# Performance work log

Hardware: AMD Instinct MI355X
Metric: run time of the kernel (lower is better)

The kernel has to match this reference:

```python
import jax, jax.numpy as jnp
import numpy as np

N_NODES = 100000
N_EDGES = 3200000
IN_F, HID, OUT_F = 256, 128, 8


def gcn_conv(x, src, dst, W, b, n_nodes):
    # PyG GCNConv: linear transform, add self-loops, symmetric normalization, scatter-add, bias
    x = x @ W  # [N, F_out]
    loop = jnp.arange(n_nodes, dtype=src.dtype)
    src_f = jnp.concatenate([src, loop])
    dst_f = jnp.concatenate([dst, loop])
    ones = jnp.ones(src_f.shape[0], dtype=x.dtype)
    deg = jax.ops.segment_sum(ones, dst_f, num_segments=n_nodes)  # in-degree incl self-loop
    dinv = jax.lax.rsqrt(jnp.maximum(deg, 1e-12))
    norm = dinv[src_f] * dinv[dst_f]  # [E+N]
    msgs = x[src_f] * norm[:, None]
    out = jax.ops.segment_sum(msgs, dst_f, num_segments=n_nodes)
    return out + b


def setup_inputs() -> dict:
    key = jax.random.key(0)
    k1, k2, k3, k4 = jax.random.split(key, 4)
    x = jax.random.normal(k1, (N_NODES, IN_F), dtype=jnp.float32)
    edge_index = jax.random.randint(k2, (2, N_EDGES), 0, N_NODES, dtype=jnp.int64)
    W1 = jax.random.normal(k3, (IN_F, HID), dtype=jnp.float32) * (1.0 / np.sqrt(IN_F))
    b1 = jnp.zeros((HID,), dtype=jnp.float32)
    W2 = jax.random.normal(k4, (HID, OUT_F), dtype=jnp.float32) * (1.0 / np.sqrt(HID))
    b2 = jnp.zeros((OUT_F,), dtype=jnp.float32)
    return {"x": x, "edge_index": edge_index, "W1": W1, "b1": b1, "W2": W2, "b2": b2}


def reference(x, edge_index, W1, b1, W2, b2):
    n_nodes = x.shape[0]
    src, dst = edge_index[0], edge_index[1]
    h = gcn_conv(x, src, dst, W1, b1, n_nodes)
    h = jax.nn.relu(h)
    h = gcn_conv(h, src, dst, W2, b2, n_nodes)
    return jax.nn.log_softmax(h, axis=1)
```

## Files before the change

### kernel.cpp

```cpp
#include <hip/hip_runtime.h>
#include <hip/hip_bf16.h>
#include <stdint.h>

#define N_NODES 100000
#define N_EDGES 3200000
#define IN_F 256
#define HID 128
#define OUT_F 8

#define NB   391
#define PASS 6144
#define CAP  10240
#define BCAP 9216

typedef short short8 __attribute__((ext_vector_type(8)));
typedef float f32x4 __attribute__((ext_vector_type(4)));
typedef float f32x2 __attribute__((ext_vector_type(2)));


__device__ __forceinline__ uint32_t pk_bf16(float a, float b) {
    uint32_t ua = __float_as_uint(a);
    uint32_t ub = __float_as_uint(b);
    ua = (ua + 0x7fff + ((ua >> 16) & 1)) >> 16;
    ub = (ub + 0x7fff + ((ub >> 16) & 1)) & 0xffff0000u;
    return ua | ub;
}

__global__ __launch_bounds__(512) void k_part(const int* __restrict__ src,
                                              const int* __restrict__ dst,
                                              int* __restrict__ gcur,
                                              uint32_t* __restrict__ epk, int E) {
    __shared__ int lcntA[NB], lcntB[NB], lcnt[NB], loff[NB], ladj[NB], lcur[NB];
    __shared__ int sc[512];
    __shared__ uint32_t stage[PASS];
    int tid = threadIdx.x;
    int e0 = blockIdx.x * PASS;
    int nE = E - e0; if (nE > PASS) nE = PASS;
    int n4 = nE >> 2;

    for (int i = tid; i < NB; i += 512) { lcntA[i] = 0; lcntB[i] = 0; lcur[i] = 0; }
    __syncthreads();
    const int4* d4 = (const int4*)(dst + e0);
    const int4* s4 = (const int4*)(src + e0);
    {
        int* lc = ((tid >> 6) & 1) ? lcntB : lcntA;
        for (int i = tid; i < n4; i += 512) {
            int4 d = d4[i];
            atomicAdd(&lc[d.x >> 8], 1);
            atomicAdd(&lc[d.y >> 8], 1);
            atomicAdd(&lc[d.z >> 8], 1);
            atomicAdd(&lc[d.w >> 8], 1);
        }
    }
    __syncthreads();
    int v = 0;
    if (tid < NB) { v = lcntA[tid] + lcntB[tid]; lcnt[tid] = v; }
    sc[tid] = v;
    __syncthreads();
    for (int d = 1; d < 512; d <<= 1) {
        int t = (tid >= d) ? sc[tid - d] : 0;
        __syncthreads();
        sc[tid] += t;
        __syncthreads();
    }
    if (tid < NB) loff[tid] = sc[tid] - v;
    __syncthreads();
    if (tid < NB) {
        int len = lcnt[tid];
        if (len > 0) ladj[tid] = atomicAdd(&gcur[tid * 64], len);
    }
    __syncthreads();
    for (int i = tid; i < n4; i += 512) {
        int4 s = s4[i];
        int4 d = d4[i];
        int b0 = d.x >> 8, b1 = d.y >> 8, b2 = d.z >> 8, b3 = d.w >> 8;
        int r0 = atomicAdd(&lcur[b0], 1);
        int r1 = atomicAdd(&lcur[b1], 1);
        int r2 = atomicAdd(&lcur[b2], 1);
        int r3 = atomicAdd(&lcur[b3], 1);
        stage[loff[b0] + r0] = (uint32_t)s.x | ((uint32_t)(d.x & 255) << 17);
        stage[loff[b1] + r1] = (uint32_t)s.y | ((uint32_t)(d.y & 255) << 17);
        stage[loff[b2] + r2] = (uint32_t)s.z | ((uint32_t)(d.z & 255) << 17);
        stage[loff[b3] + r3] = (uint32_t)s.w | ((uint32_t)(d.w & 255) << 17);
    }
    __syncthreads();
    int wv = tid >> 6, ln = tid & 63;
    int sub = ln >> 4, l16 = ln & 15;
    for (int b = wv * 4 + sub; b < NB; b += 32) {
        int len = lcnt[b];
        if (len) {
            int lo = loff[b];
            uint32_t* dstp = epk + (size_t)b * BCAP + ladj[b];
            for (int j = l16; j < len; j += 16) dstp[j] = stage[lo + j];
        }
    }
}

__global__ __launch_bounds__(1024) void k_csr(const uint32_t* __restrict__ epk,
                                              const int* __restrict__ gcur,
                                              int* __restrict__ offs,
                                              int* __restrict__ cnt,
                                              float* __restrict__ dinv,
                                              int* __restrict__ ssrc, int N) {
    __shared__ int lcntP[4][256], lcur[256], loff[256];
    __shared__ uint32_t stage[CAP];
    int tid = threadIdx.x, b = blockIdx.x;
    size_t base = (size_t)b * BCAP;
    int m = gcur[b * 64];
    const uint32_t* ep = epk + base;

    if (tid < 256) { lcntP[0][tid] = 0; lcntP[1][tid] = 0; lcntP[2][tid] = 0; lcntP[3][tid] = 0; }
    __syncthreads();
    {
        int* lc = lcntP[(tid >> 6) & 3];
        for (int i = tid; i < m; i += 1024)
            atomicAdd(&lc[(ep[i] >> 17) & 255], 1);
    }
    __syncthreads();
    int v = 0;
    if (tid < 256) {
        v = lcntP[0][tid] + lcntP[1][tid] + lcntP[2][tid] + lcntP[3][tid];
        loff[tid] = v;
    }
    __syncthreads();
    for (int d = 1; d < 256; d <<= 1) {
        int t = (tid >= d && tid < 256) ? loff[tid - d] : 0;
        __syncthreads();
        if (tid < 256) loff[tid] += t;
        __syncthreads();
    }
    int excl = (tid < 256) ? (loff[tid] - v) : 0;
    __syncthreads();
    if (tid < 256) {
        loff[tid] = excl;
        lcur[tid] = 0;
        int node = b * 256 + tid;
        if (node < N) {
            offs[node] = (int)base + excl;
            cnt[node] = v;
            dinv[node] = rsqrtf((float)(v + 1));
        }
    }
    __syncthreads();
    if (m <= CAP) {
        for (int i = tid; i < m; i += 1024) {
            uint32_t u = ep[i];
            int ld = (u >> 17) & 255;
            int r = atomicAdd(&lcur[ld], 1);
            stage[loff[ld] + r] = u & 0x1FFFF;
        }
        __syncthreads();
        for (int i = tid; i < m; i += 1024) ssrc[base + i] = (int)stage[i];
    } else {
        for (int i = tid; i < m; i += 1024) {
            uint32_t u = ep[i];
            int ld = (u >> 17) & 255;
            int r = atomicAdd(&lcur[ld], 1);
            ssrc[base + loff[ld] + r] = (int)(u & 0x1FFFF);
        }
    }
}

__global__ __launch_bounds__(256) void k_wcast(const float* __restrict__ W1,
                                               ushort* __restrict__ Wbf) {
    __shared__ ushort T[128][33];
    int t = threadIdx.x;
    int k0 = blockIdx.x * 32;
    for (int idx = t; idx < 32 * 128; idx += 256) {
        int k = idx >> 7, n = idx & 127;
        uint32_t uv = __float_as_uint(W1[(size_t)(k0 + k) * HID + n]);
        uv = (uv + 0x7fff + ((uv >> 16) & 1)) >> 16;
        T[n][k] = (ushort)uv;
    }
    __syncthreads();
    for (int idx = t; idx < 32 * 128; idx += 256) {
        int n = idx >> 5, k = idx & 31;
        Wbf[(size_t)n * IN_F + k0 + k] = T[n][k];
    }
}

__global__ __launch_bounds__(256) void k_gemm1(const float* __restrict__ X,
                                               const ushort* __restrict__ Wbf,
                                               const float* __restrict__ dinv,
                                               uint32_t* __restrict__ Hs8, int M) {
    __shared__ uint32_t As[64 * 20];
    __shared__ uint32_t Bs[128 * 20];
    int t = threadIdx.x;
    int lane = t & 63, w = t >> 6;
    int q = lane >> 4, c16 = lane & 15;
    int row0 = blockIdx.x * 64;

    int ar = t >> 2, a4 = (t & 3);
    int grow = row0 + ar; if (grow >= M) grow = M - 1;
    const float* xrow = X + (size_t)grow * IN_F;
    int bn = t >> 1, b1h = (t & 1);
    const ushort* wrow = Wbf + (size_t)bn * IN_F;

    f32x4 acc[8];
    #pragma unroll
    for (int j = 0; j < 8; j++) acc[j] = (f32x4){0.f, 0.f, 0.f, 0.f};

    for (int kc = 0; kc < IN_F; kc += 32) {
        float4 x0 = *(const float4*)(xrow + kc + a4 * 8);
        float4 x1 = *(const float4*)(xrow + kc + a4 * 8 + 4);
        uint4 wv0 = *(const uint4*)(wrow + kc + b1h * 16);
        uint4 wv1 = *(const uint4*)(wrow + kc + b1h * 16 + 8);
        __syncthreads();
        *(uint2*)&As[ar * 20 + a4 * 4]     = make_uint2(pk_bf16(x0.x, x0.y), pk_bf16(x0.z, x0.w));
        *(uint2*)&As[ar * 20 + a4 * 4 + 2] = make_uint2(pk_bf16(x1.x, x1.y), pk_bf16(x1.z, x1.w));
        *(uint4*)&Bs[bn * 20 + b1h * 8]     = wv0;
        *(uint4*)&Bs[bn * 20 + b1h * 8 + 4] = wv1;
        __syncthreads();
        short8 af = *(const short8*)&As[(w * 16 + c16) * 20 + q * 4];
        #pragma unroll
        for (int j = 0; j < 8; j++) {
            short8 bf = *(const short8*)&Bs[(j * 16 + c16) * 20 + q * 4];
            acc[j] = __builtin_amdgcn_mfma_f32_16x16x32_bf16(af, bf, acc[j], 0, 0, 0);
        }
    }
    float dv[4];
    #pragma unroll
    for (int r = 0; r < 4; r++) {
        int gr = row0 + w * 16 + q * 4 + r;
        dv[r] = (gr < M) ? dinv[gr] : 0.f;
    }
    #pragma unroll
    for (int r = 0; r < 4; r++) {
        int gr = row0 + w * 16 + q * 4 + r;
        uint32_t lo = 0, hi = 0;
        lo = __builtin_amdgcn_cvt_pk_fp8_f32(acc[0][r] * dv[r], acc[1][r] * dv[r], lo, false);
        lo = __builtin_amdgcn_cvt_pk_fp8_f32(acc[2][r] * dv[r], acc[3][r] * dv[r], lo, true);
        hi = __builtin_amdgcn_cvt_pk_fp8_f32(acc[4][r] * dv[r], acc[5][r] * dv[r], hi, false);
        hi = __builtin_amdgcn_cvt_pk_fp8_f32(acc[6][r] * dv[r], acc[7][r] * dv[r], hi, true);
        if (gr < M) *(uint2*)&Hs8[(size_t)gr * 32 + c16 * 2] = make_uint2(lo, hi);
    }
}

__global__ __launch_bounds__(256) void k_agg1(const uint32_t* __restrict__ hs,
                                              const int* __restrict__ offs,
                                              const int* __restrict__ cnt,
                                              const float* __restrict__ dinv,
                                              const int* __restrict__ ssrc,
                                              const float* __restrict__ b1,
                                              const float* __restrict__ W2,
                                              uint32_t* __restrict__ h2bf, int N) {
    __shared__ float w2t[OUT_F * HID];
    __shared__ float b1p[HID];
    int t = threadIdx.x;
    for (int i = t; i < OUT_F * HID; i += 256) {
        int f = i >> 7, rem = i & 127;
        int cc = rem >> 2, bb = rem & 3;
        int feat = ((cc & 1) * 4 + bb) * 16 + (cc >> 1);
        w2t[i] = W2[feat * OUT_F + f];
    }
    if (t < HID) {
        int cc = t >> 2, bb = t & 3;
        b1p[t] = b1[((cc & 1) * 4 + bb) * 16 + (cc >> 1)];
    }
    __syncthreads();
    int wid = (blockIdx.x * 256 + t) >> 6;
    int lane = t & 63;
    if (wid >= N) return;
    int h = lane >> 5, c = lane & 31;
    float dv = dinv[wid];
    f32x2 s01 = {0.f, 0.f}, s23 = {0.f, 0.f};
    if (h == 0) {
        uint32_t u = hs[(size_t)wid * 32 + c];
        s01 = __builtin_amdgcn_cvt_pk_f32_fp8(u, false);
        s23 = __builtin_amdgcn_cvt_pk_f32_fp8(u, true);
    }
    int beg = offs[wid], n = cnt[wid];
    const int* sp = ssrc + beg;
    int j = h;
    for (; j + 14 < n; j += 16) {
        int e0 = sp[j],      e1 = sp[j + 2],  e2 = sp[j + 4],  e3 = sp[j + 6];
        int e4 = sp[j + 8],  e5 = sp[j + 10], e6 = sp[j + 12], e7 = sp[j + 14];
        uint32_t u0 = hs[(size_t)e0 * 32 + c];
        uint32_t u1 = hs[(size_t)e1 * 32 + c];
        uint32_t u2 = hs[(size_t)e2 * 32 + c];
        uint32_t u3 = hs[(size_t)e3 * 32 + c];
        uint32_t u4 = hs[(size_t)e4 * 32 + c];
        uint32_t u5 = hs[(size_t)e5 * 32 + c];
        uint32_t u6 = hs[(size_t)e6 * 32 + c];
        uint32_t u7 = hs[(size_t)e7 * 32 + c];
        s01 += __builtin_amdgcn_cvt_pk_f32_fp8(u0, false); s23 += __builtin_amdgcn_cvt_pk_f32_fp8(u0, true);
        s01 += __builtin_amdgcn_cvt_pk_f32_fp8(u1, false); s23 += __builtin_amdgcn_cvt_pk_f32_fp8(u1, true);
        s01 += __builtin_amdgcn_cvt_pk_f32_fp8(u2, false); s23 += __builtin_amdgcn_cvt_pk_f32_fp8(u2, true);
        s01 += __builtin_amdgcn_cvt_pk_f32_fp8(u3, false); s23 += __builtin_amdgcn_cvt_pk_f32_fp8(u3, true);
        s01 += __builtin_amdgcn_cvt_pk_f32_fp8(u4, false); s23 += __builtin_amdgcn_cvt_pk_f32_fp8(u4, true);
        s01 += __builtin_amdgcn_cvt_pk_f32_fp8(u5, false); s23 += __builtin_amdgcn_cvt_pk_f32_fp8(u5, true);
        s01 += __builtin_amdgcn_cvt_pk_f32_fp8(u6, false); s23 += __builtin_amdgcn_cvt_pk_f32_fp8(u6, true);
        s01 += __builtin_amdgcn_cvt_pk_f32_fp8(u7, false); s23 += __builtin_amdgcn_cvt_pk_f32_fp8(u7, true);
    }
    for (; j + 6 < n; j += 8) {
        int e0 = sp[j], e1 = sp[j + 2], e2 = sp[j + 4], e3 = sp[j + 6];
        uint32_t u0 = hs[(size_t)e0 * 32 + c];
        uint32_t u1 = hs[(size_t)e1 * 32 + c];
        uint32_t u2 = hs[(size_t)e2 * 32 + c];
        uint32_t u3 = hs[(size_t)e3 * 32 + c];
        s01 += __builtin_amdgcn_cvt_pk_f32_fp8(u0, false); s23 += __builtin_amdgcn_cvt_pk_f32_fp8(u0, true);
        s01 += __builtin_amdgcn_cvt_pk_f32_fp8(u1, false); s23 += __builtin_amdgcn_cvt_pk_f32_fp8(u1, true);
        s01 += __builtin_amdgcn_cvt_pk_f32_fp8(u2, false); s23 += __builtin_amdgcn_cvt_pk_f32_fp8(u2, true);
        s01 += __builtin_amdgcn_cvt_pk_f32_fp8(u3, false); s23 += __builtin_amdgcn_cvt_pk_f32_fp8(u3, true);
    }
    for (; j < n; j += 2) {
        uint32_t u = hs[(size_t)sp[j] * 32 + c];
        s01 += __builtin_amdgcn_cvt_pk_f32_fp8(u, false);
        s23 += __builtin_amdgcn_cvt_pk_f32_fp8(u, true);
    }
    s01[0] += __shfl_xor(s01[0], 32);
    s01[1] += __shfl_xor(s01[1], 32);
    s23[0] += __shfl_xor(s23[0], 32);
    s23[1] += __shfl_xor(s23[1], 32);
    float4 bb = *(const float4*)(b1p + c * 4);
    float o0 = fmaxf(fmaf(s01[0], dv, bb.x), 0.f);
    float o1 = fmaxf(fmaf(s01[1], dv, bb.y), 0.f);
    float o2 = fmaxf(fmaf(s23[0], dv, bb.z), 0.f);
    float o3 = fmaxf(fmaf(s23[1], dv, bb.w), 0.f);
    int f0 = h * 4;
    float p[4];
    #pragma unroll
    for (int f = 0; f < 4; f++) {
        float4 wv = *(const float4*)&w2t[(f0 + f) * HID + c * 4];
        p[f] = o0 * wv.x + o1 * wv.y + o2 * wv.z + o3 * wv.w;
    }
    #pragma unroll
    for (int d = 1; d < 32; d <<= 1) {
        #pragma unroll
        for (int f = 0; f < 4; f++) p[f] += __shfl_xor(p[f], d);
    }
    if (c == 0) {
        uint32_t w0 = pk_bf16(p[0] * dv, p[1] * dv);
        uint32_t w1 = pk_bf16(p[2] * dv, p[3] * dv);
        *(uint2*)&h2bf[(size_t)wid * 4 + h * 2] = make_uint2(w0, w1);
    }
}

__global__ __launch_bounds__(256) void k_agg2(const uint32_t* __restrict__ h2bf,
                                              const int* __restrict__ offs,
                                              const int* __restrict__ cnt,
                                              const float* __restrict__ dinv,
                                              const int* __restrict__ ssrc,
                                              const float* __restrict__ b2,
                                              float* __restrict__ out, int N) {
    int wid = (blockIdx.x * 256 + threadIdx.x) >> 6;
    int lane = threadIdx.x & 63;
    if (wid >= N) return;
    int f2 = lane & 3, g = lane >> 2;
    float dv = dinv[wid];
    int beg = offs[wid], n = cnt[wid];
    const int* sp = ssrc + beg;
    float a0 = 0.f, a1 = 0.f;
    int j = g;
    for (; j + 48 < n; j += 64) {
        int s0 = sp[j], s1 = sp[j + 16], s2 = sp[j + 32], s3 = sp[j + 48];
        uint32_t v0 = h2bf[(size_t)s0 * 4 + f2];
        uint32_t v1 = h2bf[(size_t)s1 * 4 + f2];
        uint32_t v2 = h2bf[(size_t)s2 * 4 + f2];
        uint32_t v3 = h2bf[(size_t)s3 * 4 + f2];
        a0 += __uint_as_float(v0 << 16) + __uint_as_float(v1 << 16)
            + __uint_as_float(v2 << 16) + __uint_as_float(v3 << 16);
        a1 += __uint_as_float(v0 & 0xffff0000u) + __uint_as_float(v1 & 0xffff0000u)
            + __uint_as_float(v2 & 0xffff0000u) + __uint_as_float(v3 & 0xffff0000u);
    }
    for (; j < n; j += 16) {
        uint32_t v = h2bf[(size_t)sp[j] * 4 + f2];
        a0 += __uint_as_float(v << 16);
        a1 += __uint_as_float(v & 0xffff0000u);
    }
    a0 += __shfl_xor(a0, 4);  a1 += __shfl_xor(a1, 4);
    a0 += __shfl_xor(a0, 8);  a1 += __shfl_xor(a1, 8);
    a0 += __shfl_xor(a0, 16); a1 += __shfl_xor(a1, 16);
    a0 += __shfl_xor(a0, 32); a1 += __shfl_xor(a1, 32);
    uint32_t vs = h2bf[(size_t)wid * 4 + f2];
    a0 += __uint_as_float(vs << 16);
    a1 += __uint_as_float(vs & 0xffff0000u);
    float acc0 = fmaf(a0, dv, b2[f2 * 2]);
    float acc1 = fmaf(a1, dv, b2[f2 * 2 + 1]);
    float m = fmaxf(acc0, acc1);
    m = fmaxf(m, __shfl_xor(m, 1));
    m = fmaxf(m, __shfl_xor(m, 2));
    float e = expf(acc0 - m) + expf(acc1 - m);
    e += __shfl_xor(e, 1);
    e += __shfl_xor(e, 2);
    float ls = logf(e);
    if (g == 0) {
        float2 r = make_float2(acc0 - m - ls, acc1 - m - ls);
        *(float2*)&out[(size_t)wid * OUT_F + f2 * 2] = r;
    }
}

extern "C" void kernel_launch(void* const* d_in, const int* in_sizes, int n_in,
                              void* d_out, int out_size, void* d_ws, size_t ws_size,
                              hipStream_t stream) {
    const float* x   = (const float*)d_in[0];
    const int*   ei  = (const int*)d_in[1];
    const float* W1  = (const float*)d_in[2];
    const float* b1  = (const float*)d_in[3];
    const float* W2  = (const float*)d_in[4];
    const float* b2  = (const float*)d_in[5];
    float* out = (float*)d_out;

    const int N = N_NODES, E = N_EDGES;
    const int* src = ei;
    const int* dst = ei + E;

    char* p = (char*)d_ws;
    auto carve = [&](size_t bytes) -> void* {
        void* r = (void*)p;
        p += (bytes + 511) & ~(size_t)511;
        return r;
    };
    int*      gcur  = (int*)carve((size_t)NB * 64 * 4);
    uint32_t* epk   = (uint32_t*)carve((size_t)NB * BCAP * 4);
    int*      offs  = (int*)carve((size_t)N * 4);
    int*      cnt   = (int*)carve((size_t)N * 4);
    float*    dinv  = (float*)carve((size_t)N * 4);
    int*      ssrc  = (int*)carve((size_t)NB * BCAP * 4);
    ushort*   wbf   = (ushort*)carve((size_t)HID * IN_F * 2);
    uint32_t* hs8   = (uint32_t*)carve((size_t)N * 32 * 4);
    uint32_t* h2bf  = (uint32_t*)carve((size_t)N * 4 * 4);

    hipMemsetAsync(gcur, 0, (size_t)NB * 64 * 4, stream);

    k_wcast<<<8, 256, 0, stream>>>(W1, wbf);
    k_part<<<(E + PASS - 1) / PASS, 512, 0, stream>>>(src, dst, gcur, epk, E);
    k_csr<<<NB, 1024, 0, stream>>>(epk, gcur, offs, cnt, dinv, ssrc, N);

    k_gemm1<<<(N + 63) / 64, 256, 0, stream>>>(x, wbf, dinv, hs8, N);
    k_agg1<<<(N * 64 + 255) / 256, 256, 0, stream>>>(hs8, offs, cnt, dinv, ssrc, b1, W2, h2bf, N);
    k_agg2<<<(N * 64 + 255) / 256, 256, 0, stream>>>(h2bf, offs, cnt, dinv, ssrc, b2, out, N);
}
```

Measured before the change: 345.3 us.

## Split layer-1 aggregation into four feature-slice passes with atomic partial projection

Layer-1 aggregation now runs as four sequential block passes, each gathering only a 32-byte slice of every neighbor's 128-byte fp8 row, with 8 edges in flight per wave instead of 2. The aim is to shrink the gathered working set per pass so it fits in cache better. Each pass atomically adds its partial W2 projection into a float buffer, and a new finalize kernel scales and packs that buffer to bf16. The cost is reading the index lists four times, plus an extra memset, atomics and one more kernel launch.

```diff
diff --git a/kernel.cpp b/kernel.cpp
--- a/kernel.cpp
+++ b/kernel.cpp
@@ -12,6 +12,7 @@
 #define PASS 6144
 #define CAP  10240
 #define BCAP 9216
+#define NPP  25000
 
 typedef short short8 __attribute__((ext_vector_type(8)));
 typedef float f32x4 __attribute__((ext_vector_type(4)));
@@ -236,104 +237,103 @@
     }
 }
 
-__global__ __launch_bounds__(256) void k_agg1(const uint32_t* __restrict__ hs,
-                                              const int* __restrict__ offs,
-                                              const int* __restrict__ cnt,
-                                              const float* __restrict__ dinv,
-                                              const int* __restrict__ ssrc,
-                                              const float* __restrict__ b1,
-                                              const float* __restrict__ W2,
-                                              uint32_t* __restrict__ h2bf, int N) {
-    __shared__ float w2t[OUT_F * HID];
+__global__ __launch_bounds__(256) void k_agg1p(const uint32_t* __restrict__ hs,
+                                               const int* __restrict__ offs,
+                                               const int* __restrict__ cnt,
+                                               const float* __restrict__ dinv,
+                                               const int* __restrict__ ssrc,
+                                               const float* __restrict__ b1,
+                                               const float* __restrict__ W2,
+                                               float* __restrict__ h2acc, int N) {
+    __shared__ float w2p[HID * 9];
     __shared__ float b1p[HID];
     int t = threadIdx.x;
-    for (int i = t; i < OUT_F * HID; i += 256) {
-        int f = i >> 7, rem = i & 127;
-        int cc = rem >> 2, bb = rem & 3;
+    for (int i = t; i < HID * OUT_F; i += 256) {
+        int row = i >> 3, f = i & 7;
+        int cc = row >> 2, bb = row & 3;
         int feat = ((cc & 1) * 4 + bb) * 16 + (cc >> 1);
-        w2t[i] = W2[feat * OUT_F + f];
+        w2p[row * 9 + f] = W2[feat * OUT_F + f];
     }
     if (t < HID) {
         int cc = t >> 2, bb = t & 3;
         b1p[t] = b1[((cc & 1) * 4 + bb) * 16 + (cc >> 1)];
     }
     __syncthreads();
-    int wid = (blockIdx.x * 256 + t) >> 6;
+    int pass = blockIdx.x / NPP;
+    int bid  = blockIdx.x % NPP;
+    int wid = (bid * 256 + t) >> 6;
     int lane = t & 63;
     if (wid >= N) return;
-    int h = lane >> 5, c = lane & 31;
+    int slot = lane >> 3, c8 = lane & 7;
+    int w = pass * 8 + c8;
     float dv = dinv[wid];
+    const uint32_t* hw = hs + w;
     f32x2 s01 = {0.f, 0.f}, s23 = {0.f, 0.f};
-    if (h == 0) {
-        uint32_t u = hs[(size_t)wid * 32 + c];
+    if (slot == 0) {
+        uint32_t u = hw[(size_t)wid * 32];
         s01 = __builtin_amdgcn_cvt_pk_f32_fp8(u, false);
         s23 = __builtin_amdgcn_cvt_pk_f32_fp8(u, true);
     }
     int beg = offs[wid], n = cnt[wid];
     const int* sp = ssrc + beg;
-    int j = h;
-    for (; j + 14 < n; j += 16) {
-        int e0 = sp[j],      e1 = sp[j + 2],  e2 = sp[j + 4],  e3 = sp[j + 6];
-        int e4 = sp[j + 8],  e5 = sp[j + 10], e6 = sp[j + 12], e7 = sp[j + 14];
-        uint32_t u0 = hs[(size_t)e0 * 32 + c];
-        uint32_t u1 = hs[(size_t)e1 * 32 + c];
-        uint32_t u2 = hs[(size_t)e2 * 32 + c];
-        uint32_t u3 = hs[(size_t)e3 * 32 + c];
-        uint32_t u4 = hs[(size_t)e4 * 32 + c];
-        uint32_t u5 = hs[(size_t)e5 * 32 + c];
-        uint32_t u6 = hs[(size_t)e6 * 32 + c];
-        uint32_t u7 = hs[(size_t)e7 * 32 + c];
-        s01 += __builtin_amdgcn_cvt_pk_f32_fp8(u0, false); s23 += __builtin_amdgcn_cvt_pk_f32_fp8(u0, true);
-        s01 += __builtin_amdgcn_cvt_pk_f32_fp8(u1, false); s23 += __builtin_amdgcn_cvt_pk_f32_fp8(u1, true);
-        s01 += __builtin_amdgcn_cvt_pk_f32_fp8(u2, false); s23 += __builtin_amdgcn_cvt_pk_f32_fp8(u2, true);
-        s01 += __builtin_amdgcn_cvt_pk_f32_fp8(u3, false); s23 += __builtin_amdgcn_cvt_pk_f32_fp8(u3, true);
-        s01 += __builtin_amdgcn_cvt_pk_f32_fp8(u4, false); s23 += __builtin_amdgcn_cvt_pk_f32_fp8(u4, true);
-        s01 += __builtin_amdgcn_cvt_pk_f32_fp8(u5, false); s23 += __builtin_amdgcn_cvt_pk_f32_fp8(u5, true);
-        s01 += __builtin_amdgcn_cvt_pk_f32_fp8(u6, false); s23 += __builtin_amdgcn_cvt_pk_f32_fp8(u6, true);
-        s01 += __builtin_amdgcn_cvt_pk_f32_fp8(u7, false); s23 += __builtin_amdgcn_cvt_pk_f32_fp8(u7, true);
-    }
-    for (; j + 6 < n; j += 8) {
-        int e0 = sp[j], e1 = sp[j + 2], e2 = sp[j + 4], e3 = sp[j + 6];
-        uint32_t u0 = hs[(size_t)e0 * 32 + c];
-        uint32_t u1 = hs[(size_t)e1 * 32 + c];
-        uint32_t u2 = hs[(size_t)e2 * 32 + c];
-        uint32_t u3 = hs[(size_t)e3 * 32 + c];
-        s01 += __builtin_amdgcn_cvt_pk_f32_fp8(u0, false); s23 += __builtin_amdgcn_cvt_pk_f32_fp8(u0, true);
-        s01 += __builtin_amdgcn_cvt_pk_f32_fp8(u1, false); s23 += __builtin_amdgcn_cvt_pk_f32_fp8(u1, true);
-        s01 += __builtin_amdgcn_cvt_pk_f32_fp8(u2, false); s23 += __builtin_amdgcn_cvt_pk_f32_fp8(u2, true);
-        s01 += __builtin_amdgcn_cvt_pk_f32_fp8(u3, false); s23 += __builtin_amdgcn_cvt_pk_f32_fp8(u3, true);
-    }
-    for (; j < n; j += 2) {
-        uint32_t u = hs[(size_t)sp[j] * 32 + c];
-        s01 += __builtin_amdgcn_cvt_pk_f32_fp8(u, false);
-        s23 += __builtin_amdgcn_cvt_pk_f32_fp8(u, true);
-    }
-    s01[0] += __shfl_xor(s01[0], 32);
-    s01[1] += __shfl_xor(s01[1], 32);
-    s23[0] += __shfl_xor(s23[0], 32);
-    s23[1] += __shfl_xor(s23[1], 32);
-    float4 bb = *(const float4*)(b1p + c * 4);
+#define ACC1(U) do { \
+        s01 += __builtin_amdgcn_cvt_pk_f32_fp8((U), false); \
+        s23 += __builtin_amdgcn_cvt_pk_f32_fp8((U), true);  \
+    } while (0)
+    int j = slot;
+    for (; j + 24 < n; j += 32) {
+        int e0 = sp[j], e1 = sp[j + 8], e2 = sp[j + 16], e3 = sp[j + 24];
+        uint32_t u0 = hw[(size_t)e0 * 32];
+        uint32_t u1 = hw[(size_t)e1 * 32];
+        uint32_t u2 = hw[(size_t)e2 * 32];
+        uint32_t u3 = hw[(size_t)e3 * 32];
+        ACC1(u0); ACC1(u1); ACC1(u2); ACC1(u3);
+    }
+    for (; j + 8 < n; j += 16) {
+        int e0 = sp[j], e1 = sp[j + 8];
+        uint32_t u0 = hw[(size_t)e0 * 32];
+        uint32_t u1 = hw[(size_t)e1 * 32];
+        ACC1(u0); ACC1(u1);
+    }
+    for (; j < n; j += 8) {
+        uint32_t u = hw[(size_t)sp[j] * 32];
+        ACC1(u);
+    }
+#undef ACC1
+    s01[0] += __shfl_xor(s01[0], 8);  s01[1] += __shfl_xor(s01[1], 8);
+    s23[0] += __shfl_xor(s23[0], 8);  s23[1] += __shfl_xor(s23[1], 8);
+    s01[0] += __shfl_xor(s01[0], 16); s01[1] += __shfl_xor(s01[1], 16);
+    s23[0] += __shfl_xor(s23[0], 16); s23[1] += __shfl_xor(s23[1], 16);
+    s01[0] += __shfl_xor(s01[0], 32); s01[1] += __shfl_xor(s01[1], 32);
+    s23[0] += __shfl_xor(s23[0], 32); s23[1] += __shfl_xor(s23[1], 32);
+    float4 bb = *(const float4*)&b1p[w * 4];
     float o0 = fmaxf(fmaf(s01[0], dv, bb.x), 0.f);
     float o1 = fmaxf(fmaf(s01[1], dv, bb.y), 0.f);
     float o2 = fmaxf(fmaf(s23[0], dv, bb.z), 0.f);
     float o3 = fmaxf(fmaf(s23[1], dv, bb.w), 0.f);
-    int f0 = h * 4;
-    float p[4];
+    float p[8];
     #pragma unroll
-    for (int f = 0; f < 4; f++) {
-        float4 wv = *(const float4*)&w2t[(f0 + f) * HID + c * 4];
-        p[f] = o0 * wv.x + o1 * wv.y + o2 * wv.z + o3 * wv.w;
+    for (int f = 0; f < 8; f++) {
+        p[f] = o0 * w2p[(w * 4 + 0) * 9 + f] + o1 * w2p[(w * 4 + 1) * 9 + f]
+             + o2 * w2p[(w * 4 + 2) * 9 + f] + o3 * w2p[(w * 4 + 3) * 9 + f];
     }
     #pragma unroll
-    for (int d = 1; d < 32; d <<= 1) {
+    for (int d = 1; d < 8; d <<= 1) {
         #pragma unroll
-        for (int f = 0; f < 4; f++) p[f] += __shfl_xor(p[f], d);
-    }
-    if (c == 0) {
-        uint32_t w0 = pk_bf16(p[0] * dv, p[1] * dv);
-        uint32_t w1 = pk_bf16(p[2] * dv, p[3] * dv);
-        *(uint2*)&h2bf[(size_t)wid * 4 + h * 2] = make_uint2(w0, w1);
-    }
+        for (int f = 0; f < 8; f++) p[f] += __shfl_xor(p[f], d);
+    }
+    if (slot == 0) atomicAdd(&h2acc[(size_t)wid * OUT_F + c8], p[c8]);
+}
+
+__global__ __launch_bounds__(256) void k_fin(const float* __restrict__ h2acc,
+                                             const float* __restrict__ dinv,
+                                             uint32_t* __restrict__ h2bf, int N) {
+    int i = blockIdx.x * 256 + threadIdx.x;
+    if (i >= N * 4) return;
+    int node = i >> 2;
+    float dv = dinv[node];
+    float2 v = *(const float2*)&h2acc[(size_t)i * 2];
+    h2bf[i] = pk_bf16(v.x * dv, v.y * dv);
 }
 
 __global__ __launch_bounds__(256) void k_agg2(const uint32_t* __restrict__ h2bf,
@@ -419,15 +419,18 @@
     int*      ssrc  = (int*)carve((size_t)NB * BCAP * 4);
     ushort*   wbf   = (ushort*)carve((size_t)HID * IN_F * 2);
     uint32_t* hs8   = (uint32_t*)carve((size_t)N * 32 * 4);
+    float*    h2acc = (float*)carve((size_t)N * OUT_F * 4);
     uint32_t* h2bf  = (uint32_t*)carve((size_t)N * 4 * 4);
 
     hipMemsetAsync(gcur, 0, (size_t)NB * 64 * 4, stream);
+    hipMemsetAsync(h2acc, 0, (size_t)N * OUT_F * 4, stream);
 
     k_wcast<<<8, 256, 0, stream>>>(W1, wbf);
     k_part<<<(E + PASS - 1) / PASS, 512, 0, stream>>>(src, dst, gcur, epk, E);
     k_csr<<<NB, 1024, 0, stream>>>(epk, gcur, offs, cnt, dinv, ssrc, N);
 
     k_gemm1<<<(N + 63) / 64, 256, 0, stream>>>(x, wbf, dinv, hs8, N);
-    k_agg1<<<(N * 64 + 255) / 256, 256, 0, stream>>>(hs8, offs, cnt, dinv, ssrc, b1, W2, h2bf, N);
+    k_agg1p<<<4 * NPP, 256, 0, stream>>>(hs8, offs, cnt, dinv, ssrc, b1, W2, h2acc, N);
+    k_fin<<<(N * 4 + 255) / 256, 256, 0, stream>>>(h2acc, dinv, h2bf, N);
     k_agg2<<<(N * 64 + 255) / 256, 256, 0, stream>>>(h2bf, offs, cnt, dinv, ssrc, b2, out, N);
 }
```

Measured after the change: 552.4 us. 1.6x slower.
